# Performance work log

Hardware: AMD Instinct MI355X
Metric: run time of the kernel (lower is better)

Reference implementation:

```python
import jax, jax.numpy as jnp
import numpy as np

EMB = 64
NEG = 0.2  # DGL GATConv default negative_slope

def seg_sum(x, ids, n):
    return jax.ops.segment_sum(x, ids, num_segments=n)

def seg_max(x, ids, n):
    return jax.ops.segment_max(x, ids, num_segments=n)

def gat(x, src, dst, W, al, ar):
    # DGL GATConv: fc (no bias), per-head additive attention, edge softmax over in-edges of dst
    N = x.shape[0]
    H, D = al.shape
    h = (x @ W).reshape(N, H, D)                 # (N,H,D)
    el = jnp.sum(h * al, -1)                     # (N,H)
    er = jnp.sum(h * ar, -1)                     # (N,H)
    e = jax.nn.leaky_relu(el[src] + er[dst], negative_slope=NEG)  # (E,H)
    m = seg_max(e, dst, N)
    ex = jnp.exp(e - m[dst])
    den = seg_sum(ex, dst, N)
    alpha = ex / den[dst]                        # (E,H)
    return seg_sum(alpha[..., None] * h[src], dst, N)  # (N,H,D)

def conv1d(x, w, b):
    y = jax.lax.conv_general_dilated(x, w, (1,), 'VALID', dimension_numbers=('NCH', 'OIH', 'NCH'))
    return y + b[None, :, None]

def maxpool1d(x, k, s):
    return jax.lax.reduce_window(x, -jnp.inf, jax.lax.max, (1, 1, k), (1, 1, s), 'VALID')

def textcnn(pad_dmap, c1w, c1b, c2w, c2b, c3w, c3b):
    x = jnp.squeeze(pad_dmap, 1).transpose(0, 2, 1)   # (B, emb, L)
    x = maxpool1d(conv1d(x, c1w, c1b), 3, 3)
    x = maxpool1d(conv1d(x, c2w, c2b), 3, 3)
    x = maxpool1d(conv1d(x, c3w, c3b), 130, 1)        # (B,128,1)
    return jnp.squeeze(x, 2)

def branch(feat, src, dst, nid, pad_dmap, ng, p):
    g = jax.nn.relu(gat(feat, src, dst, p['Wg1'], p['al1'], p['ar1'])).reshape(-1, EMB * 3)
    g = jax.nn.relu(gat(g, src, dst, p['Wg2'], p['al2'], p['ar2'])).reshape(-1, EMB * 9)
    g = jax.nn.relu(gat(g, src, dst, p['Wg3'], p['al3'], p['ar3'])).reshape(-1, EMB * 9)
    gmax = seg_max(g, nid, ng)                        # graph-level MaxPooling readout
    g = jax.nn.relu(gmax @ p['fcg_w'] + p['fcg_b'])
    s = textcnn(pad_dmap, p['c1w'], p['c1b'], p['c2w'], p['c2b'], p['c3w'], p['c3b'])
    s = jax.nn.relu(s @ p['tf_w'] + p['tf_b'])
    w = jax.nn.sigmoid(p['w1'])
    return (1.0 - w) * g + w * s

PKEYS = ['Wg1', 'al1', 'ar1', 'Wg2', 'al2', 'ar2', 'Wg3', 'al3', 'ar3', 'fcg_w', 'fcg_b',
         'c1w', 'c1b', 'c2w', 'c2b', 'c3w', 'c3b', 'tf_w', 'tf_b', 'w1',
         'fc1_w', 'fc1_b', 'fc2_w', 'fc2_b', 'out_w', 'out_b']

def forward(feat1, feat2, pad_dmap1, pad_dmap2, params, src1, dst1, src2, dst2, nid1, nid2, num_graphs):
    p = dict(zip(PKEYS, params))
    gc1 = branch(feat1, src1, dst1, nid1, pad_dmap1, num_graphs, p)
    gc2 = branch(feat2, src2, dst2, nid2, pad_dmap2, num_graphs, p)
    gc = jnp.concatenate([gc1, gc2], axis=1)
    gc = jax.nn.relu(gc @ p['fc1_w'] + p['fc1_b'])   # dropout is identity at eval
    gc = jax.nn.relu(gc @ p['fc2_w'] + p['fc2_b'])
    return jax.nn.sigmoid(gc @ p['out_w'] + p['out_b'])

def setup_inputs() -> dict:
    key = jax.random.key(0)
    ks = jax.random.split(key, 40)
    N, E, B, L = 8000, 160000, 16, 1200
    d = {}
    d['feat1'] = jax.random.normal(ks[0], (N, EMB), jnp.float32)
    d['feat2'] = jax.random.normal(ks[1], (N, EMB), jnp.float32)
    d['pad_dmap1'] = jax.random.normal(ks[2], (B, 1, L, EMB), jnp.float32)
    d['pad_dmap2'] = jax.random.normal(ks[3], (B, 1, L, EMB), jnp.float32)
    d['src1'] = jax.random.randint(ks[4], (E,), 0, N, jnp.int32)
    d['dst1'] = jax.random.randint(ks[5], (E,), 0, N, jnp.int32)
    d['src2'] = jax.random.randint(ks[6], (E,), 0, N, jnp.int32)
    d['dst2'] = jax.random.randint(ks[7], (E,), 0, N, jnp.int32)
    nid = ((jnp.arange(N) * B) // N).astype(jnp.int32)  # sorted, all graphs non-empty
    d['nid1'] = nid
    d['nid2'] = nid
    d['num_graphs'] = B
    def lin(k, i, o):
        return jax.random.normal(k, (i, o), jnp.float32) * np.float32(1.0 / np.sqrt(i))
    d['Wg1'] = lin(ks[8], EMB, EMB * 3)
    d['al1'] = jax.random.normal(ks[9], (3, EMB), jnp.float32) * 0.1
    d['ar1'] = jax.random.normal(ks[10], (3, EMB), jnp.float32) * 0.1
    d['Wg2'] = lin(ks[11], EMB * 3, EMB * 9)
    d['al2'] = jax.random.normal(ks[12], (3, EMB * 3), jnp.float32) * 0.1
    d['ar2'] = jax.random.normal(ks[13], (3, EMB * 3), jnp.float32) * 0.1
    d['Wg3'] = lin(ks[14], EMB * 9, EMB * 9)
    d['al3'] = jax.random.normal(ks[15], (1, EMB * 9), jnp.float32) * 0.1
    d['ar3'] = jax.random.normal(ks[16], (1, EMB * 9), jnp.float32) * 0.1
    d['fcg_w'] = lin(ks[17], EMB * 9, 128)
    d['fcg_b'] = jnp.zeros((128,), jnp.float32)
    d['c1w'] = jax.random.normal(ks[18], (128, EMB, 3), jnp.float32) * np.float32(1.0 / np.sqrt(EMB * 3))
    d['c1b'] = jnp.zeros((128,), jnp.float32)
    d['c2w'] = jax.random.normal(ks[19], (128, 128, 3), jnp.float32) * np.float32(1.0 / np.sqrt(128 * 3))
    d['c2b'] = jnp.zeros((128,), jnp.float32)
    d['c3w'] = jax.random.normal(ks[20], (128, 128, 3), jnp.float32) * np.float32(1.0 / np.sqrt(128 * 3))
    d['c3b'] = jnp.zeros((128,), jnp.float32)
    d['tf_w'] = lin(ks[21], 128, 128)
    d['tf_b'] = jnp.zeros((128,), jnp.float32)
    d['w1'] = jnp.full((1,), 0.5, jnp.float32)
    d['fc1_w'] = lin(ks[22], 256, 512)
    d['fc1_b'] = jnp.zeros((512,), jnp.float32)
    d['fc2_w'] = lin(ks[23], 512, 256)
    d['fc2_b'] = jnp.zeros((256,), jnp.float32)
    d['out_w'] = lin(ks[24], 256, 1)
    d['out_b'] = jnp.zeros((1,), jnp.float32)
    return d

def reference(feat1, src1, dst1, nid1, pad_dmap1, feat2, src2, dst2, nid2, pad_dmap2, num_graphs,
              Wg1, al1, ar1, Wg2, al2, ar2, Wg3, al3, ar3, fcg_w, fcg_b,
              c1w, c1b, c2w, c2b, c3w, c3b, tf_w, tf_b, w1,
              fc1_w, fc1_b, fc2_w, fc2_b, out_w, out_b):
    params = (Wg1, al1, ar1, Wg2, al2, ar2, Wg3, al3, ar3, fcg_w, fcg_b,
              c1w, c1b, c2w, c2b, c3w, c3b, tf_w, tf_b, w1,
              fc1_w, fc1_b, fc2_w, fc2_b, out_w, out_b)
    return forward(feat1, feat2, pad_dmap1, pad_dmap2, params, src1, dst1, src2, dst2, nid1, nid2, num_graphs)
```

## Files before the change

### kernel.cpp

```cpp
#include <hip/hip_runtime.h>
#include <hip/hip_bf16.h>
#include <math.h>

#define NEG_SLOPE 0.2f

__global__ void zero_i32(int* __restrict__ p, int n) {
    int i = blockIdx.x * blockDim.x + threadIdx.x;
    if (i < n) p[i] = 0;
}

__global__ void count_edges2(const int* __restrict__ dst0, const int* __restrict__ dst1,
                             int* __restrict__ cnt, int N, int E) {
    int i = blockIdx.x * blockDim.x + threadIdx.x;
    if (i >= 2 * E) return;
    int br = i >= E;
    int j = i - br * E;
    const int* d = br ? dst1 : dst0;
    atomicAdd(&cnt[br * N + d[j]], 1);
}

__global__ void scan_block(int* __restrict__ cnt_all, int* __restrict__ rs_all, int N) {
    __shared__ int s[1024];
    int br = blockIdx.x;
    int* cnt = cnt_all + br * N;
    int* rs = rs_all + br * (N + 1);
    int tid = threadIdx.x;
    int running = 0;
    for (int base = 0; base < N; base += 1024) {
        int v = (base + tid < N) ? cnt[base + tid] : 0;
        if (base + tid < N) cnt[base + tid] = 0;
        __syncthreads();
        s[tid] = v;
        __syncthreads();
        for (int off = 1; off < 1024; off <<= 1) {
            int t = (tid >= off) ? s[tid - off] : 0;
            __syncthreads();
            if (tid >= off) s[tid] += t;
            __syncthreads();
        }
        if (base + tid < N) rs[base + tid] = running + s[tid] - v;
        running += s[1023];
    }
    if (tid == 0) rs[N] = running;
}

__global__ void scatter_edges2(const int* __restrict__ dst0, const int* __restrict__ dst1,
                               const int* __restrict__ rs_all, int* __restrict__ fill_all,
                               int* __restrict__ eidx_all, int N, int E) {
    int i = blockIdx.x * blockDim.x + threadIdx.x;
    if (i >= 2 * E) return;
    int br = i >= E;
    int j = i - br * E;
    const int* d = br ? dst1 : dst0;
    int dd = d[j];
    int pos = atomicAdd(&fill_all[br * N + dd], 1);
    eidx_all[br * E + rs_all[br * (N + 1) + dd] + pos] = j;
}

__device__ __forceinline__ short f2bf(float x) {
    __hip_bfloat16 h = __float2bfloat16(x);
    return *reinterpret_cast<short*>(&h);
}
__device__ __forceinline__ float bf2f(short s) {
    unsigned int u = ((unsigned int)(unsigned short)s) << 16;
    return __uint_as_float(u);
}
__device__ __forceinline__ float us2f(unsigned short s) {
    return __uint_as_float((unsigned int)s << 16);
}

__device__ __forceinline__ void split_w_elem(const float* W, short* W2t, int K, int N, int idx) {
    int k = idx / N, n = idx - k * N;
    float x = W[idx];
    short hs = f2bf(x);
    short ls = f2bf(x - bf2f(hs));
    size_t base = (size_t)n * 2 * K;
    W2t[base + k] = hs;
    W2t[base + K + k] = ls;
}
__device__ __forceinline__ void split_cw_elem(const float* w, short* w2, int Kp, int idx) {
    int o = idx / Kp, k = idx - o * Kp;
    float x = w[idx];
    short hs = f2bf(x);
    short ls = f2bf(x - bf2f(hs));
    size_t base = (size_t)o * 2 * Kp;
    w2[base + k] = hs;
    w2[base + Kp + k] = ls;
}
__global__ void prep_weights(const float* __restrict__ Wg1, const float* __restrict__ Wg2,
                             const float* __restrict__ Wg3, const float* __restrict__ c1w,
                             const float* __restrict__ c2w, const float* __restrict__ c3w,
                             short* __restrict__ w2t1, short* __restrict__ w2t2,
                             short* __restrict__ w2t3, short* __restrict__ cw1,
                             short* __restrict__ cw2, short* __restrict__ cw3) {
    int idx = blockIdx.x * blockDim.x + threadIdx.x;
    if (idx < 12288)       split_w_elem(Wg1, w2t1, 64, 192, idx);
    else if (idx < 122880) split_w_elem(Wg2, w2t2, 192, 576, idx - 12288);
    else if (idx < 454656) split_w_elem(Wg3, w2t3, 576, 576, idx - 122880);
    else if (idx < 479232) split_cw_elem(c1w, cw1, 192, idx - 454656);
    else if (idx < 528384) split_cw_elem(c2w, cw2, 384, idx - 479232);
    else if (idx < 577536) split_cw_elem(c3w, cw3, 384, idx - 528384);
}

typedef __attribute__((ext_vector_type(8))) short short8;
typedef __attribute__((ext_vector_type(4))) short short4v;
typedef __attribute__((ext_vector_type(4))) float floatx4;

__global__ __launch_bounds__(256) void gemm_bf3_v4(const float* __restrict__ A0,
                                                   const float* __restrict__ A1,
                                                   const short* __restrict__ Bt,
                                                   unsigned short* __restrict__ Cbf,
                                                   int M, int K, int N, size_t cBrStride) {
    __shared__ __align__(16) short sA[64 * 72];
    __shared__ __align__(16) short sB[192 * 72];
    int tid = threadIdx.x;
    int wave = tid >> 6, lane = tid & 63;
    int m = lane & 15, q = lane >> 4;
    int row0 = blockIdx.y << 6;
    int col0 = blockIdx.x * 192;
    const float* A = blockIdx.z ? A1 : A0;
    unsigned short* Cbfb = Cbf + blockIdx.z * cBrStride;
    int K2 = K * 2;
    floatx4 acc[4][3];
#pragma unroll
    for (int rt = 0; rt < 4; ++rt)
#pragma unroll
        for (int ct = 0; ct < 3; ++ct) acc[rt][ct] = (floatx4){0.f, 0.f, 0.f, 0.f};

    for (int k0 = 0; k0 < K; k0 += 32) {
#pragma unroll
        for (int p = 0; p < 2; ++p) {
            int t = tid + (p << 8);
            int r = t >> 3, c = (t & 7) << 2;
            float4 av = *(const float4*)&A[(size_t)(row0 + r) * K + k0 + c];
            short4v hs, ls;
            hs[0] = f2bf(av.x); ls[0] = f2bf(av.x - bf2f(hs[0]));
            hs[1] = f2bf(av.y); ls[1] = f2bf(av.y - bf2f(hs[1]));
            hs[2] = f2bf(av.z); ls[2] = f2bf(av.z - bf2f(hs[2]));
            hs[3] = f2bf(av.w); ls[3] = f2bf(av.w - bf2f(hs[3]));
            *(short4v*)&sA[r * 72 + c] = hs;
            *(short4v*)&sA[r * 72 + 32 + c] = ls;
        }
#pragma unroll
        for (int p = 0; p < 6; ++p) {
            int t = tid + (p << 8);
            int n = t >> 3, sub = t & 7;
            int srcoff = k0 + (sub << 3) + ((sub >= 4) ? (K - 32) : 0);
            *(float4*)&sB[n * 72 + (sub << 3)] =
                *(const float4*)&Bt[(size_t)(col0 + n) * K2 + srcoff];
        }
        __syncthreads();
        short8 a_hi[4], a_lo[4];
#pragma unroll
        for (int rt = 0; rt < 4; ++rt) {
            a_hi[rt] = *(const short8*)&sA[(rt * 16 + m) * 72 + q * 8];
            a_lo[rt] = *(const short8*)&sA[(rt * 16 + m) * 72 + 32 + q * 8];
        }
#pragma unroll
        for (int ct = 0; ct < 3; ++ct) {
            short8 b_hi = *(const short8*)&sB[(wave * 48 + ct * 16 + m) * 72 + q * 8];
            short8 b_lo = *(const short8*)&sB[(wave * 48 + ct * 16 + m) * 72 + 32 + q * 8];
#pragma unroll
            for (int rt = 0; rt < 4; ++rt) {
                acc[rt][ct] = __builtin_amdgcn_mfma_f32_16x16x32_bf16(a_hi[rt], b_hi, acc[rt][ct], 0, 0, 0);
                acc[rt][ct] = __builtin_amdgcn_mfma_f32_16x16x32_bf16(a_lo[rt], b_hi, acc[rt][ct], 0, 0, 0);
                acc[rt][ct] = __builtin_amdgcn_mfma_f32_16x16x32_bf16(a_hi[rt], b_lo, acc[rt][ct], 0, 0, 0);
            }
        }
        __syncthreads();
    }
#pragma unroll
    for (int rt = 0; rt < 4; ++rt)
#pragma unroll
        for (int ct = 0; ct < 3; ++ct)
#pragma unroll
            for (int r = 0; r < 4; ++r) {
                size_t idx = (size_t)(row0 + rt * 16 + q * 4 + r) * N + col0 + wave * 48 + ct * 16 + m;
                Cbfb[idx] = (unsigned short)f2bf(acc[rt][ct][r]);
            }
}

__global__ void gat_elr(const unsigned short* __restrict__ h, const float* __restrict__ al,
                        const float* __restrict__ ar, float* __restrict__ el,
                        float* __restrict__ er, int N, int H, int D,
                        size_t hBr, size_t eBr) {
    int wid = (blockIdx.x * blockDim.x + threadIdx.x) >> 6;
    int lane = threadIdx.x & 63;
    if (wid >= 2 * N * H) return;
    int br = wid / (N * H);
    int loc = wid - br * N * H;
    int n = loc / H, hh = loc - n * H;
    const unsigned short* hp = h + br * hBr + ((size_t)n * H + hh) * D;
    const float* alp = al + (size_t)hh * D;
    const float* arp = ar + (size_t)hh * D;
    float sl = 0.f, sr = 0.f;
    for (int d = lane; d < D; d += 64) {
        float v = us2f(hp[d]);
        sl += v * alp[d];
        sr += v * arp[d];
    }
    for (int off = 32; off > 0; off >>= 1) {
        sl += __shfl_down(sl, off, 64);
        sr += __shfl_down(sr, off, 64);
    }
    if (lane == 0) { el[br * eBr + loc] = sl; er[br * eBr + loc] = sr; }
}

__device__ __forceinline__ float lrelu(float v) {
    return (v > 0.f) ? v : NEG_SLOPE * v;
}

#define TILE_E 64
__global__ void gat_softagg(const unsigned short* __restrict__ hb_all,
                            const float* __restrict__ el_all, const float* __restrict__ er_all,
                            const int* __restrict__ src0, const int* __restrict__ src1,
                            const int* __restrict__ rs_all, const int* __restrict__ eidx_all,
                            float4* __restrict__ out4_all, int N, int H, int D, int E,
                            size_t hBr, size_t eBr, size_t o4Br) {
    __shared__ int s_src[TILE_E];
    __shared__ float s_alpha[TILE_E * 3];
    __shared__ float s_stat[6];
    int n = blockIdx.x;
    int br = blockIdx.y;
    const int* src = br ? src1 : src0;
    const int* rs = rs_all + br * (N + 1);
    const int* eidx = eidx_all + br * E;
    const unsigned short* hb = hb_all + br * hBr;
    const float* el = el_all + br * eBr;
    const float* er = er_all + br * eBr;
    float4* out4 = out4_all + br * o4Br;
    int HD = H * D;
    int HD4 = HD >> 2;
    int tid = threadIdx.x;
    int s0 = rs[n], s1 = rs[n + 1];
    int deg = s1 - s0;
    bool activeC = tid < HD4;
    int hh = activeC ? (tid << 2) / D : 0;
    float4 accA = {0.f, 0.f, 0.f, 0.f};
    float4 accB = {0.f, 0.f, 0.f, 0.f};

    if (deg > 0 && deg <= 64) {
        if (tid < 64) {
            int lane = tid;
            float ern0 = er[n * H + 0];
            float ern1 = (H > 1) ? er[n * H + 1] : 0.f;
            float ern2 = (H > 2) ? er[n * H + 2] : 0.f;
            int s = 0;
            float v0 = -INFINITY, v1 = -INFINITY, v2 = -INFINITY;
            if (lane < deg) {
                int e = eidx[s0 + lane];
                s = src[e];
                v0 = lrelu(el[s * H + 0] + ern0);
                if (H > 1) {
                    v1 = lrelu(el[s * H + 1] + ern1);
                    v2 = lrelu(el[s * H + 2] + ern2);
                }
            }
            float m0 = v0, m1 = v1, m2 = v2;
#pragma unroll
            for (int off = 32; off > 0; off >>= 1) {
                m0 = fmaxf(m0, __shfl_xor(m0, off, 64));
                m1 = fmaxf(m1, __shfl_xor(m1, off, 64));
                m2 = fmaxf(m2, __shfl_xor(m2, off, 64));
            }
            float ex0 = (lane < deg) ? expf(v0 - m0) : 0.f;
            float ex1 = (lane < deg && H > 1) ? expf(v1 - m1) : 0.f;
            float ex2 = (lane < deg && H > 2) ? expf(v2 - m2) : 0.f;
            float d0 = ex0, d1 = ex1, d2 = ex2;
#pragma unroll
            for (int off = 32; off > 0; off >>= 1) {
                d0 += __shfl_xor(d0, off, 64);
                d1 += __shfl_xor(d1, off, 64);
                d2 += __shfl_xor(d2, off, 64);
            }
            if (lane < deg) {
                s_src[lane] = s;
                s_alpha[lane * 3 + 0] = ex0 / d0;
                if (H > 1) {
                    s_alpha[lane * 3 + 1] = ex1 / d1;
                    s_alpha[lane * 3 + 2] = ex2 / d2;
                }
            }
        }
        __syncthreads();
        if (activeC) {
            int i = 0;
#pragma unroll 4
            for (; i + 1 < deg; i += 2) {
                float a0 = s_alpha[i * 3 + hh];
                float a1 = s_alpha[(i + 1) * 3 + hh];
                ushort4 h0 = *(const ushort4*)&hb[(size_t)s_src[i] * HD + (tid << 2)];
                ushort4 h1 = *(const ushort4*)&hb[(size_t)s_src[i + 1] * HD + (tid << 2)];
                accA.x += a0 * us2f(h0.x); accA.y += a0 * us2f(h0.y);
                accA.z += a0 * us2f(h0.z); accA.w += a0 * us2f(h0.w);
                accB.x += a1 * us2f(h1.x); accB.y += a1 * us2f(h1.y);
                accB.z += a1 * us2f(h1.z); accB.w += a1 * us2f(h1.w);
            }
            if (i < deg) {
                float a0 = s_alpha[i * 3 + hh];
                ushort4 h0 = *(const ushort4*)&hb[(size_t)s_src[i] * HD + (tid << 2)];
                accA.x += a0 * us2f(h0.x); accA.y += a0 * us2f(h0.y);
                accA.z += a0 * us2f(h0.z); accA.w += a0 * us2f(h0.w);
            }
        }
    } else if (deg > 64) {
        if (tid < 64) {
            int lane = tid;
            float ern0 = er[n * H + 0];
            float ern1 = (H > 1) ? er[n * H + 1] : 0.f;
            float ern2 = (H > 2) ? er[n * H + 2] : 0.f;
            float m0 = -INFINITY, m1 = -INFINITY, m2 = -INFINITY;
            for (int j = s0 + lane; j < s1; j += 64) {
                int e = eidx[j], s = src[e];
                m0 = fmaxf(m0, lrelu(el[s * H + 0] + ern0));
                if (H > 1) {
                    m1 = fmaxf(m1, lrelu(el[s * H + 1] + ern1));
                    m2 = fmaxf(m2, lrelu(el[s * H + 2] + ern2));
                }
            }
#pragma unroll
            for (int off = 32; off > 0; off >>= 1) {
                m0 = fmaxf(m0, __shfl_xor(m0, off, 64));
                m1 = fmaxf(m1, __shfl_xor(m1, off, 64));
                m2 = fmaxf(m2, __shfl_xor(m2, off, 64));
            }
            float d0 = 0.f, d1 = 0.f, d2 = 0.f;
            for (int j = s0 + lane; j < s1; j += 64) {
                int e = eidx[j], s = src[e];
                d0 += expf(lrelu(el[s * H + 0] + ern0) - m0);
                if (H > 1) {
                    d1 += expf(lrelu(el[s * H + 1] + ern1) - m1);
                    d2 += expf(lrelu(el[s * H + 2] + ern2) - m2);
                }
            }
#pragma unroll
            for (int off = 32; off > 0; off >>= 1) {
                d0 += __shfl_xor(d0, off, 64);
                d1 += __shfl_xor(d1, off, 64);
                d2 += __shfl_xor(d2, off, 64);
            }
            if (lane == 0) {
                s_stat[0] = m0; s_stat[1] = m1; s_stat[2] = m2;
                s_stat[3] = 1.f / d0;
                s_stat[4] = (H > 1) ? 1.f / d1 : 0.f;
                s_stat[5] = (H > 2) ? 1.f / d2 : 0.f;
            }
        }
        __syncthreads();
        float m0 = s_stat[0], m1 = s_stat[1], m2 = s_stat[2];
        float i0 = s_stat[3], i1 = s_stat[4], i2 = s_stat[5];
        for (int base = s0; base < s1; base += TILE_E) {
            int cnt = s1 - base; if (cnt > TILE_E) cnt = TILE_E;
            __syncthreads();
            if (tid < cnt) {
                int e = eidx[base + tid], s = src[e];
                s_src[tid] = s;
                s_alpha[tid * 3 + 0] = expf(lrelu(el[s * H + 0] + er[n * H + 0]) - m0) * i0;
                if (H > 1) {
                    s_alpha[tid * 3 + 1] = expf(lrelu(el[s * H + 1] + er[n * H + 1]) - m1) * i1;
                    s_alpha[tid * 3 + 2] = expf(lrelu(el[s * H + 2] + er[n * H + 2]) - m2) * i2;
                }
            }
            __syncthreads();
            if (activeC) {
                int i = 0;
#pragma unroll 2
                for (; i + 1 < cnt; i += 2) {
                    float a0 = s_alpha[i * 3 + hh];
                    float a1 = s_alpha[(i + 1) * 3 + hh];
                    ushort4 h0 = *(const ushort4*)&hb[(size_t)s_src[i] * HD + (tid << 2)];
                    ushort4 h1 = *(const ushort4*)&hb[(size_t)s_src[i + 1] * HD + (tid << 2)];
                    accA.x += a0 * us2f(h0.x); accA.y += a0 * us2f(h0.y);
                    accA.z += a0 * us2f(h0.z); accA.w += a0 * us2f(h0.w);
                    accB.x += a1 * us2f(h1.x); accB.y += a1 * us2f(h1.y);
                    accB.z += a1 * us2f(h1.z); accB.w += a1 * us2f(h1.w);
                }
                if (i < cnt) {
                    float a0 = s_alpha[i * 3 + hh];
                    ushort4 h0 = *(const ushort4*)&hb[(size_t)s_src[i] * HD + (tid << 2)];
                    accA.x += a0 * us2f(h0.x); accA.y += a0 * us2f(h0.y);
                    accA.z += a0 * us2f(h0.z); accA.w += a0 * us2f(h0.w);
                }
            }
        }
    }
    if (activeC) {
        float4 acc;
        acc.x = fmaxf(accA.x + accB.x, 0.f);
        acc.y = fmaxf(accA.y + accB.y, 0.f);
        acc.z = fmaxf(accA.z + accB.z, 0.f);
        acc.w = fmaxf(accA.w + accB.w, 0.f);
        out4[(size_t)n * HD4 + tid] = acc;
    }
}

__global__ void seg_max_atomic(const float* __restrict__ g_all, const int* __restrict__ nid,
                               int* __restrict__ out_all, int N, int C,
                               size_t gBr, size_t oBr) {
    int br = blockIdx.y;
    const float* g = g_all + br * gBr;
    int* out = out_all + br * oBr;
    int n0 = blockIdx.x << 5;
    int n1 = n0 + 32; if (n1 > N) n1 = N;
    if (n0 >= N) return;
    for (int c = threadIdx.x; c < C; c += blockDim.x) {
        int cur = nid[n0];
        float m = 0.f;
        for (int n = n0; n < n1; ++n) {
            int gid = nid[n];
            if (gid != cur) {
                atomicMax(&out[cur * C + c], __float_as_int(m));
                cur = gid; m = 0.f;
            }
            m = fmaxf(m, g[(size_t)n * C + c]);
        }
        atomicMax(&out[cur * C + c], __float_as_int(m));
    }
}

__global__ void linear_wave(const float* __restrict__ in, const float* __restrict__ W,
                            const float* __restrict__ bias, float* __restrict__ out,
                            int K, int O, int act, size_t inBr, size_t outBr) {
    int o = blockIdx.x * 4 + (threadIdx.x >> 6);
    int b = blockIdx.y;
    int lane = threadIdx.x & 63;
    if (o >= O) return;
    const float* ip = in + blockIdx.z * inBr + (size_t)b * K;
    float acc = 0.f;
    for (int k = lane; k < K; k += 64)
        acc += ip[k] * W[(size_t)k * O + o];
    for (int off = 32; off > 0; off >>= 1)
        acc += __shfl_down(acc, off, 64);
    if (lane == 0) {
        acc += bias[o];
        if (act == 1) acc = fmaxf(acc, 0.f);
        else if (act == 2) acc = 1.f / (1.f + expf(-acc));
        out[blockIdx.z * outBr + (size_t)b * O + o] = acc;
    }
}

__global__ void linear_cat(const float* __restrict__ gvec, const float* __restrict__ sf,
                           const float* __restrict__ w1, const float* __restrict__ W,
                           const float* __restrict__ bias, float* __restrict__ out,
                           int O, int B128) {
    int o = blockIdx.x * 4 + (threadIdx.x >> 6);
    int b = blockIdx.y;
    int lane = threadIdx.x & 63;
    if (o >= 512) return;
    float w = 1.f / (1.f + expf(-w1[0]));
    float acc = 0.f;
    for (int k = lane; k < 256; k += 64) {
        int br = k >> 7, c = k & 127;
        float v = (1.f - w) * gvec[br * B128 + b * 128 + c] + w * sf[br * B128 + b * 128 + c];
        acc += v * W[(size_t)k * 512 + o];
    }
    for (int off = 32; off > 0; off >>= 1)
        acc += __shfl_down(acc, off, 64);
    if (lane == 0)
        out[(size_t)b * 512 + o] = fmaxf(acc + bias[o], 0.f);
    (void)O;
}

__global__ void transpose_pad2(const float* __restrict__ pad0, const float* __restrict__ pad1,
                               float* __restrict__ xT, int B, int L, int C) {
    int idx = blockIdx.x * blockDim.x + threadIdx.x;
    int per = B * L * C;
    if (idx >= 2 * per) return;
    int br = idx >= per;
    int loc = idx - br * per;
    const float* pad = br ? pad1 : pad0;
    int l = loc % L;
    int c = (loc / L) % C;
    int b = loc / (L * C);
    xT[idx] = pad[((size_t)b * L + l) * C + c];
}

__global__ __launch_bounds__(256) void conv_mfma(const float* __restrict__ x,
                                                 const short* __restrict__ w2,
                                                 const float* __restrict__ bias,
                                                 float* __restrict__ y,
                                                 int Cin, int Lin, int Lout,
                                                 size_t xBr, size_t yBr) {
    extern __shared__ __align__(16) char smem[];
    float* sx = (float*)smem;
    short* sB = (short*)(smem + (size_t)Cin * 68 * 4);
    int Kp = Cin * 3;
    int K2 = Kp * 2;
    int b = blockIdx.y;
    const float* xb = x + blockIdx.z * xBr + (size_t)b * Cin * Lin;
    float* yb = y + blockIdx.z * yBr + (size_t)b * 128 * Lout;
    int l0 = blockIdx.x << 6;
    int tid = threadIdx.x;
    int wave = tid >> 6, lane = tid & 63;
    int m = lane & 15, q = lane >> 4;
    int wrow = (wave & 1) << 5;
    int wcol = (wave >> 1) << 6;
    int loadL = Lin - l0; if (loadL > 66) loadL = 66;
    for (int idx = tid; idx < Cin * loadL; idx += 256) {
        int c = idx / loadL, i = idx - c * loadL;
        sx[c * 68 + i] = xb[(size_t)c * Lin + l0 + i];
    }
    floatx4 acc[2][4];
#pragma unroll
    for (int rt = 0; rt < 2; ++rt)
#pragma unroll
        for (int ct = 0; ct < 4; ++ct) acc[rt][ct] = (floatx4){0.f, 0.f, 0.f, 0.f};

    for (int k0 = 0; k0 < Kp; k0 += 32) {
#pragma unroll
        for (int p = 0; p < 4; ++p) {
            int t = tid + (p << 8);
            int o = t >> 3, slot = t & 7;
            int srcoff = k0 + ((slot & 3) << 3) + ((slot >= 4) ? Kp : 0);
            *(float4*)&sB[o * 72 + (slot << 3)] = *(const float4*)&w2[(size_t)o * K2 + srcoff];
        }
        __syncthreads();
        short8 a_hi[2], a_lo[2];
#pragma unroll
        for (int rt = 0; rt < 2; ++rt) {
            int pos = wrow + rt * 16 + m;
#pragma unroll
            for (int kk = 0; kk < 8; ++kk) {
                int k = k0 + q * 8 + kk;
                int c = k / 3, j = k - c * 3;
                float v = sx[c * 68 + pos + j];
                short hv = f2bf(v);
                a_hi[rt][kk] = hv;
                a_lo[rt][kk] = f2bf(v - bf2f(hv));
            }
        }
#pragma unroll
        for (int ct = 0; ct < 4; ++ct) {
            short8 b_hi = *(const short8*)&sB[(wcol + ct * 16 + m) * 72 + q * 8];
            short8 b_lo = *(const short8*)&sB[(wcol + ct * 16 + m) * 72 + 32 + q * 8];
#pragma unroll
            for (int rt = 0; rt < 2; ++rt) {
                acc[rt][ct] = __builtin_amdgcn_mfma_f32_16x16x32_bf16(a_hi[rt], b_hi, acc[rt][ct], 0, 0, 0);
                acc[rt][ct] = __builtin_amdgcn_mfma_f32_16x16x32_bf16(a_lo[rt], b_hi, acc[rt][ct], 0, 0, 0);
                acc[rt][ct] = __builtin_amdgcn_mfma_f32_16x16x32_bf16(a_hi[rt], b_lo, acc[rt][ct], 0, 0, 0);
            }
        }
        __syncthreads();
    }
#pragma unroll
    for (int ct = 0; ct < 4; ++ct) {
        int o = wcol + ct * 16 + m;
        float bv = bias[o];
#pragma unroll
        for (int rt = 0; rt < 2; ++rt)
#pragma unroll
            for (int r = 0; r < 4; ++r) {
                int pos = wrow + rt * 16 + q * 4 + r;
                if (l0 + pos < Lout)
                    yb[(size_t)o * Lout + l0 + pos] = acc[rt][ct][r] + bv;
            }
    }
}

__global__ void maxpool(const float* __restrict__ y, float* __restrict__ p,
                        int BC, int Lin, int k, int s, int Lout) {
    int idx = blockIdx.x * blockDim.x + threadIdx.x;
    if (idx >= BC * Lout) return;
    int lo = idx % Lout, bc = idx / Lout;
    const float* yp = y + (size_t)bc * Lin + lo * s;
    float m = -INFINITY;
    for (int i = 0; i < k; ++i) m = fmaxf(m, yp[i]);
    p[idx] = m;
}

extern "C" void kernel_launch(void* const* d_in, const int* in_sizes, int n_in,
                              void* d_out, int out_size, void* d_ws, size_t ws_size,
                              hipStream_t stream) {
    const float* feat[2] = {(const float*)d_in[0], (const float*)d_in[1]};
    const float* pad[2]  = {(const float*)d_in[2], (const float*)d_in[3]};
    const int* src[2]    = {(const int*)d_in[4], (const int*)d_in[6]};
    const int* dst[2]    = {(const int*)d_in[5], (const int*)d_in[7]};
    const int* nid[2]    = {(const int*)d_in[8], (const int*)d_in[9]};
    const float* Wg[3]   = {(const float*)d_in[11], (const float*)d_in[14], (const float*)d_in[17]};
    const float* al[3]   = {(const float*)d_in[12], (const float*)d_in[15], (const float*)d_in[18]};
    const float* ar[3]   = {(const float*)d_in[13], (const float*)d_in[16], (const float*)d_in[19]};
    const float* fcg_w = (const float*)d_in[20]; const float* fcg_b = (const float*)d_in[21];
    const float* c1w = (const float*)d_in[22];   const float* c1b = (const float*)d_in[23];
    const float* c2w = (const float*)d_in[24];   const float* c2b = (const float*)d_in[25];
    const float* c3w = (const float*)d_in[26];   const float* c3b = (const float*)d_in[27];
    const float* tf_w = (const float*)d_in[28];  const float* tf_b = (const float*)d_in[29];
    const float* w1 = (const float*)d_in[30];
    const float* fc1_w = (const float*)d_in[31]; const float* fc1_b = (const float*)d_in[32];
    const float* fc2_w = (const float*)d_in[33]; const float* fc2_b = (const float*)d_in[34];
    const float* outw = (const float*)d_in[35];  const float* outb = (const float*)d_in[36];
    float* out = (float*)d_out;

    const int N = in_sizes[0] / 64;
    const int E = in_sizes[4];
    const int B = 16, L = 1200;
    const size_t NS = (size_t)N * 576;

    char* wsb = (char*)d_ws;
    size_t off = 0;
    auto allocB = [&](size_t bytes) -> void* {
        void* p = wsb + off;
        off += (bytes + 255) & ~(size_t)255;
        return p;
    };
    auto alloc = [&](size_t elems) -> void* { return allocB(elems * 4); };

    unsigned short* h_bf = (unsigned short*)allocB(2 * NS * 2);
    float* gA    = (float*)alloc(2 * NS);
    float* el    = (float*)alloc(2 * (size_t)N * 3);
    float* er    = (float*)alloc(2 * (size_t)N * 3);
    int* rs      = (int*)alloc(2 * (N + 1));
    int* cnt     = (int*)alloc(2 * N);
    int* eidx    = (int*)alloc(2 * E);
    int* gmax    = (int*)alloc(2 * (size_t)B * 576);
    float* gvec  = (float*)alloc(2 * (size_t)B * 128);
    float* sp    = (float*)alloc(2 * (size_t)B * 128);
    float* sf    = (float*)alloc(2 * (size_t)B * 128);
    float* f1    = (float*)alloc((size_t)B * 512);
    float* f2    = (float*)alloc((size_t)B * 256);
    short* w2t1  = (short*)allocB((size_t)192 * 2 * 64 * 2);
    short* w2t2  = (short*)allocB((size_t)576 * 2 * 192 * 2);
    short* w2t3  = (short*)allocB((size_t)576 * 2 * 576 * 2);
    short* cw1   = (short*)allocB((size_t)128 * 2 * 192 * 2);
    short* cw2   = (short*)allocB((size_t)128 * 2 * 384 * 2);
    short* cw3   = (short*)allocB((size_t)128 * 2 * 384 * 2);
    size_t tcnn_elems = 2 * ((size_t)B * 64 * L + (size_t)B * 128 * (1198 + 399 + 397 + 132 + 130));
    size_t uni_elems = 2 * NS > tcnn_elems ? 2 * NS : tcnn_elems;
    float* uni = (float*)alloc(uni_elems);
    float* gB = uni;
    float* xT = uni;
    float* y1 = xT + 2 * (size_t)B * 64 * L;
    float* p1 = y1 + 2 * (size_t)B * 128 * 1198;
    float* y2 = p1 + 2 * (size_t)B * 128 * 399;
    float* p2 = y2 + 2 * (size_t)B * 128 * 397;
    float* y3 = p2 + 2 * (size_t)B * 128 * 132;
    (void)ws_size; (void)n_in; (void)out_size;

    prep_weights<<<2256, 256, 0, stream>>>(Wg[0], Wg[1], Wg[2], c1w, c2w, c3w,
                                           w2t1, w2t2, w2t3, cw1, cw2, cw3);
    short* w2t[3] = {w2t1, w2t2, w2t3};

    zero_i32<<<(2 * N + 255) / 256, 256, 0, stream>>>(cnt, 2 * N);
    count_edges2<<<(2 * E + 255) / 256, 256, 0, stream>>>(dst[0], dst[1], cnt, N, E);
    scan_block<<<2, 1024, 0, stream>>>(cnt, rs, N);
    scatter_edges2<<<(2 * E + 255) / 256, 256, 0, stream>>>(dst[0], dst[1], rs, cnt, eidx, N, E);

    const int dims[3][3] = {{64, 3, 64}, {192, 3, 192}, {576, 1, 576}};
    float* outs[3] = {gA, gB, gA};
    const float* inp0 = feat[0];
    const float* inp1 = feat[1];
    for (int ly = 0; ly < 3; ++ly) {
        int K = dims[ly][0], H = dims[ly][1], D = dims[ly][2];
        int HD = H * D;
        gemm_bf3_v4<<<dim3(HD / 192, N / 64, 2), 256, 0, stream>>>(inp0, inp1, w2t[ly], h_bf,
                                                                   N, K, HD, NS);
        int waves2 = 2 * N * H;
        gat_elr<<<((size_t)waves2 * 64 + 255) / 256, 256, 0, stream>>>(h_bf, al[ly], ar[ly], el, er,
                                                                       N, H, D, NS, (size_t)N * 3);
        int aggThreads = (((HD >> 2) + 63) / 64) * 64;
        gat_softagg<<<dim3(N, 2), aggThreads, 0, stream>>>(
            h_bf, el, er, src[0], src[1], rs, eidx, (float4*)outs[ly],
            N, H, D, E, NS, (size_t)N * 3, NS / 4);
        inp0 = outs[ly];
        inp1 = outs[ly] + NS;
    }
    zero_i32<<<(2 * B * 576 + 255) / 256, 256, 0, stream>>>(gmax, 2 * B * 576);
    seg_max_atomic<<<dim3((N + 31) / 32, 2), 256, 0, stream>>>(gA, nid[0], gmax, N, 576,
                                                               NS, (size_t)B * 576);
    linear_wave<<<dim3(32, B, 2), 256, 0, stream>>>((const float*)gmax, fcg_w, fcg_b, gvec,
                                                    576, 128, 1, (size_t)B * 576, (size_t)B * 128);

    transpose_pad2<<<((2 * B * 64 * L) + 255) / 256, 256, 0, stream>>>(pad[0], pad[1], xT, B, L, 64);
    conv_mfma<<<dim3(19, B, 2), 256, 64 * 68 * 4 + 128 * 72 * 2, stream>>>(
        xT, cw1, c1b, y1, 64, 1200, 1198, (size_t)B * 64 * L, (size_t)B * 128 * 1198);
    maxpool<<<(2 * B * 128 * 399 + 255) / 256, 256, 0, stream>>>(y1, p1, 2 * B * 128, 1198, 3, 3, 399);
    conv_mfma<<<dim3(7, B, 2), 256, 128 * 68 * 4 + 128 * 72 * 2, stream>>>(
        p1, cw2, c2b, y2, 128, 399, 397, (size_t)B * 128 * 399, (size_t)B * 128 * 397);
    maxpool<<<(2 * B * 128 * 132 + 255) / 256, 256, 0, stream>>>(y2, p2, 2 * B * 128, 397, 3, 3, 132);
    conv_mfma<<<dim3(3, B, 2), 256, 128 * 68 * 4 + 128 * 72 * 2, stream>>>(
        p2, cw3, c3b, y3, 128, 132, 130, (size_t)B * 128 * 132, (size_t)B * 128 * 130);
    maxpool<<<(2 * B * 128 + 255) / 256, 256, 0, stream>>>(y3, sp, 2 * B * 128, 130, 130, 1, 1);
    linear_wave<<<dim3(32, B, 2), 256, 0, stream>>>(sp, tf_w, tf_b, sf, 128, 128, 1,
                                                    (size_t)B * 128, (size_t)B * 128);

    linear_cat<<<dim3(128, B, 1), 256, 0, stream>>>(gvec, sf, w1, fc1_w, fc1_b, f1, 512, B * 128);
    linear_wave<<<dim3(64, B, 1), 256, 0, stream>>>(f1, fc2_w, fc2_b, f2, 512, 256, 1, 0, 0);
    linear_wave<<<dim3(1, B, 1), 256, 0, stream>>>(f2, outw, outb, out, 256, 1, 2, 0, 0);
}
```

Before: 585.8 us.

## Fuse transpose and maxpools into conv input loads; fuse final pool with linear

Removes the separate transpose kernel by reading the padded embedding map directly in (L,C) layout inside the first conv's shared-memory load. The two stride-3 maxpools are folded into the next conv's input staging, which now computes a max over three values while loading. The global max-pool and the tf linear layer are merged into one small kernel. Together these cut several launches and intermediate buffers at the cost of some redundant reads in the conv loaders and a serial 128-wide loop in the new pool+linear kernel.

```diff
diff --git a/kernel.cpp b/kernel.cpp
--- a/kernel.cpp
+++ b/kernel.cpp
@@ -461,25 +461,13 @@
     (void)O;
 }
 
-__global__ void transpose_pad2(const float* __restrict__ pad0, const float* __restrict__ pad1,
-                               float* __restrict__ xT, int B, int L, int C) {
-    int idx = blockIdx.x * blockDim.x + threadIdx.x;
-    int per = B * L * C;
-    if (idx >= 2 * per) return;
-    int br = idx >= per;
-    int loc = idx - br * per;
-    const float* pad = br ? pad1 : pad0;
-    int l = loc % L;
-    int c = (loc / L) % C;
-    int b = loc / (L * C);
-    xT[idx] = pad[((size_t)b * L + l) * C + c];
-}
-
 __global__ __launch_bounds__(256) void conv_mfma(const float* __restrict__ x,
+                                                 const float* __restrict__ x1,
                                                  const short* __restrict__ w2,
                                                  const float* __restrict__ bias,
                                                  float* __restrict__ y,
                                                  int Cin, int Lin, int Lout,
+                                                 int mode, int srcLen,
                                                  size_t xBr, size_t yBr) {
     extern __shared__ __align__(16) char smem[];
     float* sx = (float*)smem;
@@ -487,7 +475,6 @@
     int Kp = Cin * 3;
     int K2 = Kp * 2;
     int b = blockIdx.y;
-    const float* xb = x + blockIdx.z * xBr + (size_t)b * Cin * Lin;
     float* yb = y + blockIdx.z * yBr + (size_t)b * 128 * Lout;
     int l0 = blockIdx.x << 6;
     int tid = threadIdx.x;
@@ -496,9 +483,25 @@
     int wrow = (wave & 1) << 5;
     int wcol = (wave >> 1) << 6;
     int loadL = Lin - l0; if (loadL > 66) loadL = 66;
-    for (int idx = tid; idx < Cin * loadL; idx += 256) {
-        int c = idx / loadL, i = idx - c * loadL;
-        sx[c * 68 + i] = xb[(size_t)c * Lin + l0 + i];
+    if (mode == 2) {
+        const float* pb = (blockIdx.z ? x1 : x) + (size_t)b * 1200 * 64;
+        for (int t = tid; t < loadL * 64; t += 256) {
+            int i = t >> 6, c = t & 63;
+            sx[c * 68 + i] = pb[(size_t)(l0 + i) * 64 + c];
+        }
+    } else if (mode == 1) {
+        const float* xb = x + blockIdx.z * xBr + (size_t)b * Cin * srcLen;
+        for (int t = tid; t < Cin * loadL; t += 256) {
+            int c = t / loadL, i = t - c * loadL;
+            const float* row = &xb[(size_t)c * srcLen + 3 * (l0 + i)];
+            sx[c * 68 + i] = fmaxf(fmaxf(row[0], row[1]), row[2]);
+        }
+    } else {
+        const float* xb = x + blockIdx.z * xBr + (size_t)b * Cin * srcLen;
+        for (int t = tid; t < Cin * loadL; t += 256) {
+            int c = t / loadL, i = t - c * loadL;
+            sx[c * 68 + i] = xb[(size_t)c * srcLen + l0 + i];
+        }
     }
     floatx4 acc[2][4];
 #pragma unroll
@@ -557,15 +560,21 @@
     }
 }
 
-__global__ void maxpool(const float* __restrict__ y, float* __restrict__ p,
-                        int BC, int Lin, int k, int s, int Lout) {
-    int idx = blockIdx.x * blockDim.x + threadIdx.x;
-    if (idx >= BC * Lout) return;
-    int lo = idx % Lout, bc = idx / Lout;
-    const float* yp = y + (size_t)bc * Lin + lo * s;
-    float m = -INFINITY;
-    for (int i = 0; i < k; ++i) m = fmaxf(m, yp[i]);
-    p[idx] = m;
+__global__ void pooltf(const float* __restrict__ y3, const float* __restrict__ tf_w,
+                       const float* __restrict__ tf_b, float* __restrict__ sf,
+                       size_t yBr, size_t sfBr) {
+    __shared__ float s_sp[128];
+    int b = blockIdx.x, br = blockIdx.y;
+    const float* yb = y3 + br * yBr + (size_t)b * 128 * 130;
+    int c = threadIdx.x;
+    float mx = -INFINITY;
+    for (int l = 0; l < 130; ++l) mx = fmaxf(mx, yb[(size_t)c * 130 + l]);
+    s_sp[c] = mx;
+    __syncthreads();
+    int o = threadIdx.x;
+    float acc = tf_b[o];
+    for (int k = 0; k < 128; ++k) acc += s_sp[k] * tf_w[(size_t)k * 128 + o];
+    sf[br * sfBr + (size_t)b * 128 + o] = fmaxf(acc, 0.f);
 }
 
 extern "C" void kernel_launch(void* const* d_in, const int* in_sizes, int n_in,
@@ -613,7 +622,6 @@
     int* eidx    = (int*)alloc(2 * E);
     int* gmax    = (int*)alloc(2 * (size_t)B * 576);
     float* gvec  = (float*)alloc(2 * (size_t)B * 128);
-    float* sp    = (float*)alloc(2 * (size_t)B * 128);
     float* sf    = (float*)alloc(2 * (size_t)B * 128);
     float* f1    = (float*)alloc((size_t)B * 512);
     float* f2    = (float*)alloc((size_t)B * 256);
@@ -623,16 +631,13 @@
     short* cw1   = (short*)allocB((size_t)128 * 2 * 192 * 2);
     short* cw2   = (short*)allocB((size_t)128 * 2 * 384 * 2);
     short* cw3   = (short*)allocB((size_t)128 * 2 * 384 * 2);
-    size_t tcnn_elems = 2 * ((size_t)B * 64 * L + (size_t)B * 128 * (1198 + 399 + 397 + 132 + 130));
+    size_t tcnn_elems = 2 * (size_t)B * 128 * (1198 + 397 + 130);
     size_t uni_elems = 2 * NS > tcnn_elems ? 2 * NS : tcnn_elems;
     float* uni = (float*)alloc(uni_elems);
     float* gB = uni;
-    float* xT = uni;
-    float* y1 = xT + 2 * (size_t)B * 64 * L;
-    float* p1 = y1 + 2 * (size_t)B * 128 * 1198;
-    float* y2 = p1 + 2 * (size_t)B * 128 * 399;
-    float* p2 = y2 + 2 * (size_t)B * 128 * 397;
-    float* y3 = p2 + 2 * (size_t)B * 128 * 132;
+    float* y1 = uni;
+    float* y2 = y1 + 2 * (size_t)B * 128 * 1198;
+    float* y3 = y2 + 2 * (size_t)B * 128 * 397;
     (void)ws_size; (void)n_in; (void)out_size;
 
     prep_weights<<<2256, 256, 0, stream>>>(Wg[0], Wg[1], Wg[2], c1w, c2w, c3w,
@@ -669,18 +674,17 @@
     linear_wave<<<dim3(32, B, 2), 256, 0, stream>>>((const float*)gmax, fcg_w, fcg_b, gvec,
                                                     576, 128, 1, (size_t)B * 576, (size_t)B * 128);
 
-    transpose_pad2<<<((2 * B * 64 * L) + 255) / 256, 256, 0, stream>>>(pad[0], pad[1], xT, B, L, 64);
     conv_mfma<<<dim3(19, B, 2), 256, 64 * 68 * 4 + 128 * 72 * 2, stream>>>(
-        xT, cw1, c1b, y1, 64, 1200, 1198, (size_t)B * 64 * L, (size_t)B * 128 * 1198);
-    maxpool<<<(2 * B * 128 * 399 + 255) / 256, 256, 0, stream>>>(y1, p1, 2 * B * 128, 1198, 3, 3, 399);
+        pad[0], pad[1], cw1, c1b, y1, 64, 1200, 1198, 2, 0,
+        0, (size_t)B * 128 * 1198);
     conv_mfma<<<dim3(7, B, 2), 256, 128 * 68 * 4 + 128 * 72 * 2, stream>>>(
-        p1, cw2, c2b, y2, 128, 399, 397, (size_t)B * 128 * 399, (size_t)B * 128 * 397);
-    maxpool<<<(2 * B * 128 * 132 + 255) / 256, 256, 0, stream>>>(y2, p2, 2 * B * 128, 397, 3, 3, 132);
+        y1, nullptr, cw2, c2b, y2, 128, 399, 397, 1, 1198,
+        (size_t)B * 128 * 1198, (size_t)B * 128 * 397);
     conv_mfma<<<dim3(3, B, 2), 256, 128 * 68 * 4 + 128 * 72 * 2, stream>>>(
-        p2, cw3, c3b, y3, 128, 132, 130, (size_t)B * 128 * 132, (size_t)B * 128 * 130);
-    maxpool<<<(2 * B * 128 + 255) / 256, 256, 0, stream>>>(y3, sp, 2 * B * 128, 130, 130, 1, 1);
-    linear_wave<<<dim3(32, B, 2), 256, 0, stream>>>(sp, tf_w, tf_b, sf, 128, 128, 1,
-                                                    (size_t)B * 128, (size_t)B * 128);
+        y2, nullptr, cw3, c3b, y3, 128, 132, 130, 1, 397,
+        (size_t)B * 128 * 397, (size_t)B * 128 * 130);
+    pooltf<<<dim3(B, 2), 128, 0, stream>>>(y3, tf_w, tf_b, sf,
+                                           (size_t)B * 128 * 130, (size_t)B * 128);
 
     linear_cat<<<dim3(128, B, 1), 256, 0, stream>>>(gvec, sf, w1, fc1_w, fc1_b, f1, 512, B * 128);
     linear_wave<<<dim3(64, B, 1), 256, 0, stream>>>(f1, fc2_w, fc2_b, f2, 512, 256, 1, 0, 0);
```

Measured after the change: 557.1 us. -4.9%, faster.
